# Performance work log

Measured on AMD Instinct MI355X. Metric: run time of the kernel, lower is better.

The kernel has to match this reference:

```python
import jax, jax.numpy as jnp
import numpy as np

B, N, H, D, MAXH, MRP = 64, 197, 12, 64, 16, 14  # batch, tokens (14x14+cls), heads, head_dim, supernet max heads, max rel pos
TABLE = 2 * MRP + 2  # 30 rows per table


def setup_inputs() -> dict:
    key = jax.random.key(0)
    ks = jax.random.split(key, 5)
    x = jax.random.normal(ks[0], (B, N, 3 * D * MAXH), dtype=jnp.float32)
    mk = lambda k: (0.02 * jax.random.normal(k, (TABLE, D), dtype=jnp.float32))
    return {"x": x, "tk_v": mk(ks[1]), "tk_h": mk(ks[2]), "tv_v": mk(ks[3]), "tv_h": mk(ks[4])}


def _rel_pos_emb(table_v, table_h, n):
    # RelativePosition2D_super.forward(length_q=n, length_k=n)
    lq = n - 1
    s = int(np.sqrt(lq))  # 14
    r = jnp.arange(lq)
    dv = r[None, :] // s - r[:, None] // s
    dh = r[None, :] % s - r[:, None] % s
    iv = jnp.clip(dv, -MRP, MRP) + MRP + 1
    ih = jnp.clip(dh, -MRP, MRP) + MRP + 1
    iv = jnp.pad(iv, ((1, 0), (1, 0)))  # CLS row/col -> index 0
    ih = jnp.pad(ih, ((1, 0), (1, 0)))
    return table_v[iv] + table_h[ih]  # (n, n, D)


def reference(x, tk_v, tk_h, tv_v, tv_h):
    scale = D ** (-0.5)  # sample_scale = 64**-0.5
    xs = x[:, :, : H * D * 3]
    qkv = xs.reshape(B, N, 3, H, D).transpose(2, 0, 3, 1, 4)  # (3,B,H,N,D)
    q, k, v = qkv[0], qkv[1], qkv[2]
    attn = jnp.einsum('bhid,bhjd->bhij', q, k) * scale
    rk = _rel_pos_emb(tk_v, tk_h, N)  # (N,N,D)
    attn = attn + jnp.einsum('bhid,ijd->bhij', q, rk) * scale
    attn = jax.nn.softmax(attn, axis=-1)  # attn_drop p=0.0 -> identity
    out = jnp.einsum('bhij,bhjd->bhid', attn, v)
    rv = _rel_pos_emb(tv_v, tv_h, N)  # (N,N,D)
    out = out + jnp.einsum('bhij,ijd->bhid', attn, rv)
    out = out.transpose(0, 2, 1, 3).reshape(B, N, H * D)  # (B,N,768)
    return jnp.pad(out, ((0, 0), (0, 0), (0, MAXH * D - H * D)))  # pad to (B,N,1024)
```

## Files before the change

### kernel.cpp

```cpp
#include <hip/hip_runtime.h>

typedef float  f4v   __attribute__((ext_vector_type(4)));
typedef float  f32x4 __attribute__((ext_vector_type(4)));
typedef short  s8v   __attribute__((ext_vector_type(8)));
typedef short  s4v   __attribute__((ext_vector_type(4)));
typedef __bf16 bf16x8 __attribute__((ext_vector_type(8)));

#define N_   197
#define H_   12
#define CIN  3072
#define COUT 1024
#define VSTR 296
#define ASTR 72

#define MEMBAR() asm volatile("" ::: "memory")

__device__ __forceinline__ unsigned short f2bf(float f) {
    unsigned u = __float_as_uint(f);
    u += 0x7FFFu + ((u >> 16) & 1u);
    return (unsigned short)(u >> 16);
}
__device__ __forceinline__ float bf2f(unsigned short s) {
    return __uint_as_float(((unsigned)s) << 16);
}
__device__ __forceinline__ f32x4 mfma_bf16(s8v a, s8v b, f32x4 c) {
    return __builtin_amdgcn_mfma_f32_16x16x32_bf16(
        __builtin_bit_cast(bf16x8, a), __builtin_bit_cast(bf16x8, b), c, 0, 0, 0);
}
__device__ __forceinline__ void st4f(volatile unsigned short* p, float a, float b, float c, float d) {
    s4v v;
    v[0] = (short)f2bf(a); v[1] = (short)f2bf(b);
    v[2] = (short)f2bf(c); v[3] = (short)f2bf(d);
    *(volatile s4v*)p = v;
}
__device__ __forceinline__ void st4z(volatile unsigned short* p) {
    s4v v = {0, 0, 0, 0};
    *(volatile s4v*)p = v;
}

__launch_bounds__(1024, 4)
__global__ void attn_super(const float* __restrict__ x,
                           const float* __restrict__ tkv,
                           const float* __restrict__ tkh,
                           const float* __restrict__ tvv,
                           const float* __restrict__ tvh,
                           float* __restrict__ out) {
    __shared__ __align__(16) unsigned short Kl[272 * 72];
    __shared__ __align__(16) unsigned short Vt[64 * VSTR];
    __shared__ __align__(16) unsigned short AR[16][16 * ASTR];
    __shared__ __align__(16) unsigned short INDv[16 * 224];
    __shared__ __align__(16) unsigned short INDh[16 * 224];

    const int bid = blockIdx.x;
    const int b = bid / H_, h = bid % H_;
    const int tid = threadIdx.x;
    const int w  = tid >> 6;
    const int l  = tid & 63;
    const int lg = l >> 4;
    const int ln = l & 15;

    const float* xb = x + (size_t)b * N_ * CIN;

    if (h < 4) {
        float* oz = out + (size_t)b * N_ * COUT + 768 + h * 64;
        for (int idx = tid; idx < N_ * 16; idx += 1024) {
            int row = idx >> 4, c4 = idx & 15;
            f4v z = {0.f, 0.f, 0.f, 0.f};
            *(f4v*)(oz + (size_t)row * COUT + c4 * 4) = z;
        }
    }

    f4v kr[5];
    #pragma unroll
    for (int it = 0; it < 5; ++it) {
        int idx = it * 1024 + tid;
        bool a5 = (it < 4) || (tid < 256);
        int row = idx >> 4, d0 = (idx & 15) * 4;
        f4v v = {0.f, 0.f, 0.f, 0.f};
        if (a5) {
            if (row < N_)                     v = *(const f4v*)(xb + (size_t)row * CIN + 768 + h * 64 + d0);
            else if (row >= 208 && row < 238) v = *(const f4v*)(tkv + (row - 208) * 64 + d0);
            else if (row >= 240 && row < 270) v = *(const f4v*)(tkh + (row - 240) * 64 + d0);
        }
        kr[it] = v;
    }
    f4v q1[2], q2[2];
    if (w < 13) {
        int qrow = w * 16 + ln; if (qrow > 196) qrow = 196;
        const float* qp = xb + (size_t)qrow * CIN + h * 64;
        #pragma unroll
        for (int s2 = 0; s2 < 2; ++s2) {
            q1[s2] = *(const f4v*)(qp + s2 * 32 + lg * 8);
            q2[s2] = *(const f4v*)(qp + s2 * 32 + lg * 8 + 4);
        }
    }
    f4v vr[5];
    #pragma unroll
    for (int it = 0; it < 5; ++it) {
        int idx = it * 1024 + tid;
        bool a5 = (it < 4) || (tid < 512);
        int j = idx % 288, d0 = (idx / 288) * 4;
        f4v v = {0.f, 0.f, 0.f, 0.f};
        if (a5) {
            if (j < N_)                     v = *(const f4v*)(xb + (size_t)j * CIN + 1536 + h * 64 + d0);
            else if (j >= 224 && j < 254)   v = *(const f4v*)(tvv + (j - 224) * 64 + d0);
            else if (j >= 256 && j < 286)   v = *(const f4v*)(tvh + (j - 256) * 64 + d0);
        }
        vr[it] = v;
    }

    #pragma unroll
    for (int it = 0; it < 5; ++it) {
        int idx = it * 1024 + tid;
        bool a5 = (it < 4) || (tid < 256);
        if (a5) {
            int row = idx >> 4, d0 = (idx & 15) * 4;
            f4v v = kr[it];
            s4v pk;
            pk[0] = (short)f2bf(v[0]); pk[1] = (short)f2bf(v[1]);
            pk[2] = (short)f2bf(v[2]); pk[3] = (short)f2bf(v[3]);
            *(s4v*)(&Kl[row * 72 + d0]) = pk;
        }
    }
    for (int idx = tid; idx < 16 * 224; idx += 1024) {
        int m = idx / 224, k = idx % 224;
        int km1 = k - 1;
        bool kv = (k >= 1 && k <= 196);
        INDv[idx] = (kv && (km1 / 14) == m) ? (unsigned short)0x3F80 : (unsigned short)0;
        INDh[idx] = (kv && (km1 % 14) == m) ? (unsigned short)0x3F80 : (unsigned short)0;
    }
    __syncthreads();

    const int tile = w, qb = tile * 16;
    const unsigned short* ar = &AR[w][0];
    volatile unsigned short* arv = &AR[w][0];

    f32x4 S[13];
    if (w < 13) {
        s8v aq[2];
        #pragma unroll
        for (int s2 = 0; s2 < 2; ++s2) {
            #pragma unroll
            for (int e = 0; e < 4; ++e) {
                aq[s2][e]     = (short)f2bf(q1[s2][e] * 0.125f);
                aq[s2][e + 4] = (short)f2bf(q2[s2][e] * 0.125f);
            }
        }
        #pragma unroll
        for (int ct = 0; ct < 13; ++ct) {
            f32x4 acc = {0.f, 0.f, 0.f, 0.f};
            #pragma unroll
            for (int s2 = 0; s2 < 2; ++s2) {
                const s8v bk = *(const s8v*)(&Kl[(ct * 16 + ln) * 72 + s2 * 32 + lg * 8]);
                acc = mfma_bf16(bk, aq[s2], acc);
            }
            S[ct] = acc;
        }
        #pragma unroll
        for (int tt = 0; tt < 4; ++tt) {
            f32x4 acc = {0.f, 0.f, 0.f, 0.f};
            #pragma unroll
            for (int s2 = 0; s2 < 2; ++s2) {
                const s8v bk = *(const s8v*)(&Kl[((13 + tt) * 16 + ln) * 72 + s2 * 32 + lg * 8]);
                acc = mfma_bf16(bk, aq[s2], acc);
            }
            st4f(&arv[ln * ASTR + tt * 16 + 4 * lg], acc[0], acc[1], acc[2], acc[3]);
        }
    }
    #pragma unroll
    for (int it = 0; it < 5; ++it) {
        int idx = it * 1024 + tid;
        bool a5 = (it < 4) || (tid < 512);
        if (a5) {
            int j = idx % 288, d0 = (idx / 288) * 4;
            f4v v = vr[it];
            #pragma unroll
            for (int e = 0; e < 4; ++e)
                Vt[(d0 + e) * VSTR + j] = f2bf(v[e]);
        }
    }

    float rsq[4], p0q[4];
    int ritq[4], citq[4];
    if (w < 13) {
        MEMBAR();
        if (tile == 0) {
            unsigned short c0  = ar[0];
            unsigned short c32 = ar[32];
            if (l >= 15 && l <= 28) arv[l] = c0;
            if (l >= 47 && l <= 60) arv[l] = c32;
        }
        MEMBAR();
        const int iL  = qb + ln;
        const int im1 = (iL > 0) ? iL - 1 : 0;
        const int rit = im1 / 14;
        const int cit = im1 - rit * 14;
        float rs4[4] = {0.f, 0.f, 0.f, 0.f};
        #pragma unroll
        for (int ct = 0; ct < 13; ++ct) {
            int mj[4], cj[4];
            if (ct == 0) {
                #pragma unroll
                for (int r = 0; r < 4; ++r) {
                    int km1 = 4 * lg + r - 1;
                    int w14 = (km1 >= 14) ? 1 : 0;
                    mj[r] = w14; cj[r] = km1 - 14 * w14;
                }
            } else {
                unsigned e0 = (unsigned)(ct * 16 - 1 + 4 * lg);
                unsigned m0 = e0 / 14u;
                unsigned c0 = e0 - m0 * 14u;
                #pragma unroll
                for (int r = 0; r < 4; ++r) {
                    unsigned c = c0 + (unsigned)r;
                    int wr = (c >= 14u) ? 1 : 0;
                    mj[r] = (int)m0 + wr; cj[r] = (int)c - 14 * wr;
                }
            }
            #pragma unroll
            for (int r = 0; r < 4; ++r) {
                int t = mj[r] - rit + 15;
                int u = cj[r] - cit + 47;
                if (ct == 0 && r == 0) {
                    bool z = (lg == 0);
                    t = z ? 0 : t;
                    u = z ? 32 : u;
                }
                float bias = bf2f(ar[ln * ASTR + t]) + bf2f(ar[ln * ASTR + u]);
                float p = __expf(S[ct][r] + bias);
                if (ct == 12) { if (4 * lg + r > 4) p = 0.f; }
                S[ct][r] = p;
                rs4[r] += p;
            }
        }
        float rs = (rs4[0] + rs4[1]) + (rs4[2] + rs4[3]);
        rs += __shfl_xor(rs, 16);
        rs += __shfl_xor(rs, 32);
        float p00 = S[0][0];
        #pragma unroll
        for (int r = 0; r < 4; ++r) {
            rsq[r] = __shfl(rs,  4 * lg + r);
            p0q[r] = __shfl(p00, 4 * lg + r);
        }
        #pragma unroll
        for (int r = 0; r < 4; ++r) {
            int qr2 = qb + 4 * lg + r;
            int im  = (qr2 > 0) ? qr2 - 1 : 0;
            ritq[r] = im / 14;
            citq[r] = im - ritq[r] * 14;
        }
    }
    __syncthreads();

    if (w >= 13) return;

    f32x4 oacc[4];
    #pragma unroll
    for (int nt = 0; nt < 4; ++nt) { f32x4 z = {0.f,0.f,0.f,0.f}; oacc[nt] = z; }
    f32x4 cwv = {0.f,0.f,0.f,0.f}, cwh = {0.f,0.f,0.f,0.f};

    #pragma unroll
    for (int win = 0; win < 3; ++win) {
        MEMBAR();
        #pragma unroll
        for (int cc = 0; cc < 4; ++cc) {
            int ct = win * 4 + cc;
            st4f(&arv[ln * ASTR + cc * 16 + 4 * lg], S[ct][0], S[ct][1], S[ct][2], S[ct][3]);
        }
        MEMBAR();
        #pragma unroll
        for (int kk = 0; kk < 2; ++kk) {
            int kt = win * 2 + kk;
            const s8v ap = *(const s8v*)(&ar[ln * ASTR + kk * 32 + lg * 8]);
            #pragma unroll
            for (int nt = 0; nt < 4; ++nt) {
                const s8v bv = *(const s8v*)(&Vt[(nt * 16 + ln) * VSTR + kt * 32 + lg * 8]);
                oacc[nt] = mfma_bf16(ap, bv, oacc[nt]);
            }
            const s8v bi = *(const s8v*)(&INDv[ln * 224 + kt * 32 + lg * 8]);
            cwv = mfma_bf16(ap, bi, cwv);
            const s8v bh = *(const s8v*)(&INDh[ln * 224 + kt * 32 + lg * 8]);
            cwh = mfma_bf16(ap, bh, cwh);
        }
    }
    {
        MEMBAR();
        st4f(&arv[ln * ASTR + 4 * lg], S[12][0], S[12][1], S[12][2], S[12][3]);
        st4z(&arv[ln * ASTR + 16 + 4 * lg]);
        st4z(&arv[ln * ASTR + 32 + lg * 8]);
        st4z(&arv[ln * ASTR + 36 + lg * 8]);
        MEMBAR();
        {
            const s8v ap = *(const s8v*)(&ar[ln * ASTR + lg * 8]);
            #pragma unroll
            for (int nt = 0; nt < 4; ++nt) {
                const s8v bv = *(const s8v*)(&Vt[(nt * 16 + ln) * VSTR + 192 + lg * 8]);
                oacc[nt] = mfma_bf16(ap, bv, oacc[nt]);
            }
            const s8v bi = *(const s8v*)(&INDv[ln * 224 + 192 + lg * 8]);
            cwv = mfma_bf16(ap, bi, cwv);
            const s8v bh = *(const s8v*)(&INDh[ln * 224 + 192 + lg * 8]);
            cwh = mfma_bf16(ap, bh, cwh);
        }
        MEMBAR();
        #pragma unroll
        for (int r = 0; r < 4; ++r) {
            int q = 4 * lg + r;
            bool isRow0 = (tile == 0) && (q == 0);
            if (ln <= 13 && !isRow0)
                arv[q * ASTR + 47 + ln - ritq[r]] = f2bf(cwv[r]);
            if (ln == 15)
                arv[q * ASTR + 32] = f2bf(isRow0 ? rsq[r] : p0q[r]);
        }
        MEMBAR();
        {
            const s8v ap = *(const s8v*)(&ar[ln * ASTR + 32 + lg * 8]);
            #pragma unroll
            for (int nt = 0; nt < 4; ++nt) {
                const s8v bv = *(const s8v*)(&Vt[(nt * 16 + ln) * VSTR + 224 + lg * 8]);
                oacc[nt] = mfma_bf16(ap, bv, oacc[nt]);
            }
        }
    }
    {
        MEMBAR();
        st4z(&arv[ln * ASTR + lg * 8]);
        st4z(&arv[ln * ASTR + 4 + lg * 8]);
        MEMBAR();
        #pragma unroll
        for (int r = 0; r < 4; ++r) {
            int q = 4 * lg + r;
            bool isRow0 = (tile == 0) && (q == 0);
            if (ln <= 13 && !isRow0)
                arv[q * ASTR + 15 + ln - citq[r]] = f2bf(cwh[r]);
            if (ln == 15)
                arv[q * ASTR + 0] = f2bf(isRow0 ? rsq[r] : p0q[r]);
        }
        MEMBAR();
        {
            const s8v ap = *(const s8v*)(&ar[ln * ASTR + lg * 8]);
            #pragma unroll
            for (int nt = 0; nt < 4; ++nt) {
                const s8v bv = *(const s8v*)(&Vt[(nt * 16 + ln) * VSTR + 256 + lg * 8]);
                oacc[nt] = mfma_bf16(ap, bv, oacc[nt]);
            }
        }
    }
    #pragma unroll
    for (int r = 0; r < 4; ++r) {
        int n = qb + 4 * lg + r;
        if (n < N_) {
            float sc = 1.0f / rsq[r];
            float* orow = out + ((size_t)b * N_ + n) * COUT + h * 64;
            #pragma unroll
            for (int nt = 0; nt < 4; ++nt)
                orow[nt * 16 + ln] = oacc[nt][r] * sc;
        }
    }
}

extern "C" void kernel_launch(void* const* d_in, const int* in_sizes, int n_in,
                              void* d_out, int out_size, void* d_ws, size_t ws_size,
                              hipStream_t stream) {
    const float* x   = (const float*)d_in[0];
    const float* tkv = (const float*)d_in[1];
    const float* tkh = (const float*)d_in[2];
    const float* tvv = (const float*)d_in[3];
    const float* tvh = (const float*)d_in[4];
    float* o = (float*)d_out;
    attn_super<<<dim3(64 * H_), dim3(1024), 0, stream>>>(x, tkv, tkh, tvv, tvh, o);
}
```

Baseline: 75.34 us.

## Fold relative-position key bias into score MFMA via one-hot expansion matrix

Instead of gathering the per-query relative-position bias from LDS with index arithmetic for every score element, each query row's bias vector is compacted into a 32-entry, query-shifted layout. A constant one-hot matrix Bext, built in shared memory, expands that vector across keys through one extra MFMA per column tile, so the bias lands directly in the score accumulator. This removes the per-element index computation and two LDS gathers in the softmax loop. In exchange it adds one MFMA per tile, scattered bf16 stores, and about 18KB more LDS, which may reduce occupancy.

After: 71.65 us. 4.9% less time.

```diff
diff --git a/kernel.cpp b/kernel.cpp
--- a/kernel.cpp
+++ b/kernel.cpp
@@ -12,6 +12,7 @@
 #define COUT 1024
 #define VSTR 296
 #define ASTR 72
+#define BSTR 40
 
 #define MEMBAR() asm volatile("" ::: "memory")
 
@@ -50,6 +51,7 @@
     __shared__ __align__(16) unsigned short AR[16][16 * ASTR];
     __shared__ __align__(16) unsigned short INDv[16 * 224];
     __shared__ __align__(16) unsigned short INDh[16 * 224];
+    __shared__ __align__(16) unsigned short Bext[224 * BSTR];
 
     const int bid = blockIdx.x;
     const int b = bid / H_, h = bid % H_;
@@ -129,6 +131,17 @@
         INDv[idx] = (kv && (km1 / 14) == m) ? (unsigned short)0x3F80 : (unsigned short)0;
         INDh[idx] = (kv && (km1 % 14) == m) ? (unsigned short)0x3F80 : (unsigned short)0;
     }
+    for (int idx = tid; idx < 224 * 32; idx += 1024) {
+        int k = idx >> 5, c = idx & 31;
+        unsigned short v = 0;
+        if (k >= 1 && k <= 196) {
+            int mj = (k - 1) / 14, cj = (k - 1) - mj * 14;
+            if (c == mj || c == 16 + cj) v = (unsigned short)0x3F80;
+        } else if (k == 0) {
+            if (c == 15 || c == 31) v = (unsigned short)0x3F80;
+        }
+        Bext[k * BSTR + c] = v;
+    }
     __syncthreads();
 
     const int tile = w, qb = tile * 16;
@@ -136,7 +149,14 @@
     volatile unsigned short* arv = &AR[w][0];
 
     f32x4 S[13];
+    float rsq[4], p0q[4];
+    int ritq[4], citq[4];
     if (w < 13) {
+        const int iL  = qb + ln;
+        const int im1 = (iL > 0) ? iL - 1 : 0;
+        const int rit = im1 / 14;
+        const int cit = im1 - rit * 14;
+
         s8v aq[2];
         #pragma unroll
         for (int s2 = 0; s2 < 2; ++s2) {
@@ -146,25 +166,55 @@
                 aq[s2][e + 4] = (short)f2bf(q2[s2][e] * 0.125f);
             }
         }
+        float spv = 0.f, sph = 0.f;
+        #pragma unroll
+        for (int tt = 0; tt < 4; ++tt) {
+            f32x4 acc = {0.f, 0.f, 0.f, 0.f};
+            #pragma unroll
+            for (int s2 = 0; s2 < 2; ++s2) {
+                const s8v bk = *(const s8v*)(&Kl[((13 + tt) * 16 + ln) * 72 + s2 * 32 + lg * 8]);
+                acc = mfma_bf16(bk, aq[s2], acc);
+            }
+            const bool isV  = (tt < 2);
+            const int mbase = (tt & 1) * 16;
+            const int shift = isV ? rit : cit;
+            const int cbase = isV ? 0 : 16;
+            const bool skip0 = (tile == 0 && ln == 0);
+            #pragma unroll
+            for (int r = 0; r < 4; ++r) {
+                int m = mbase + 4 * lg + r;
+                int t = m + shift - 15;
+                if (!skip0 && m < 30 && t >= 0 && t < 15)
+                    arv[ln * ASTR + cbase + t] = f2bf(acc[r]);
+                if (!skip0 && m == 0)
+                    arv[ln * ASTR + cbase + 15] = f2bf(acc[r]);
+            }
+            if (tile == 0 && l == 0) {
+                if (tt == 0) spv = acc[0];
+                if (tt == 2) sph = acc[0];
+            }
+        }
+        if (tile == 0 && l == 0) {
+            unsigned short v0 = f2bf(spv), h0 = f2bf(sph);
+            #pragma unroll
+            for (int t = 0; t < 16; ++t) {
+                arv[t] = v0;
+                arv[16 + t] = h0;
+            }
+        }
+        MEMBAR();
+        const s8v aq2 = *(const s8v*)(&ar[ln * ASTR + lg * 8]);
         #pragma unroll
         for (int ct = 0; ct < 13; ++ct) {
+            const s8v be = *(const s8v*)(&Bext[(ct * 16 + ln) * BSTR + lg * 8]);
             f32x4 acc = {0.f, 0.f, 0.f, 0.f};
+            acc = mfma_bf16(be, aq2, acc);
             #pragma unroll
             for (int s2 = 0; s2 < 2; ++s2) {
                 const s8v bk = *(const s8v*)(&Kl[(ct * 16 + ln) * 72 + s2 * 32 + lg * 8]);
                 acc = mfma_bf16(bk, aq[s2], acc);
             }
             S[ct] = acc;
-        }
-        #pragma unroll
-        for (int tt = 0; tt < 4; ++tt) {
-            f32x4 acc = {0.f, 0.f, 0.f, 0.f};
-            #pragma unroll
-            for (int s2 = 0; s2 < 2; ++s2) {
-                const s8v bk = *(const s8v*)(&Kl[((13 + tt) * 16 + ln) * 72 + s2 * 32 + lg * 8]);
-                acc = mfma_bf16(bk, aq[s2], acc);
-            }
-            st4f(&arv[ln * ASTR + tt * 16 + 4 * lg], acc[0], acc[1], acc[2], acc[3]);
         }
     }
     #pragma unroll
@@ -180,54 +230,13 @@
         }
     }
 
-    float rsq[4], p0q[4];
-    int ritq[4], citq[4];
     if (w < 13) {
-        MEMBAR();
-        if (tile == 0) {
-            unsigned short c0  = ar[0];
-            unsigned short c32 = ar[32];
-            if (l >= 15 && l <= 28) arv[l] = c0;
-            if (l >= 47 && l <= 60) arv[l] = c32;
-        }
-        MEMBAR();
-        const int iL  = qb + ln;
-        const int im1 = (iL > 0) ? iL - 1 : 0;
-        const int rit = im1 / 14;
-        const int cit = im1 - rit * 14;
         float rs4[4] = {0.f, 0.f, 0.f, 0.f};
         #pragma unroll
         for (int ct = 0; ct < 13; ++ct) {
-            int mj[4], cj[4];
-            if (ct == 0) {
-                #pragma unroll
-                for (int r = 0; r < 4; ++r) {
-                    int km1 = 4 * lg + r - 1;
-                    int w14 = (km1 >= 14) ? 1 : 0;
-                    mj[r] = w14; cj[r] = km1 - 14 * w14;
-                }
-            } else {
-                unsigned e0 = (unsigned)(ct * 16 - 1 + 4 * lg);
-                unsigned m0 = e0 / 14u;
-                unsigned c0 = e0 - m0 * 14u;
-                #pragma unroll
-                for (int r = 0; r < 4; ++r) {
-                    unsigned c = c0 + (unsigned)r;
-                    int wr = (c >= 14u) ? 1 : 0;
-                    mj[r] = (int)m0 + wr; cj[r] = (int)c - 14 * wr;
-                }
-            }
             #pragma unroll
             for (int r = 0; r < 4; ++r) {
-                int t = mj[r] - rit + 15;
-                int u = cj[r] - cit + 47;
-                if (ct == 0 && r == 0) {
-                    bool z = (lg == 0);
-                    t = z ? 0 : t;
-                    u = z ? 32 : u;
-                }
-                float bias = bf2f(ar[ln * ASTR + t]) + bf2f(ar[ln * ASTR + u]);
-                float p = __expf(S[ct][r] + bias);
+                float p = __expf(S[ct][r]);
                 if (ct == 12) { if (4 * lg + r > 4) p = 0.f; }
                 S[ct][r] = p;
                 rs4[r] += p;
```
